# Kernel optimization log

Hardware: AMD Instinct MI355X
Metric: run time of the kernel (lower is better)

The kernel has to match this reference:

```python
import jax, jax.numpy as jnp
import numpy as np

B, I, D = 16384, 128, 16  # batch, input_size, n_dim


def setup_inputs() -> dict:
    key = jax.random.key(0)
    ks = jax.random.split(key, 14)
    inp = {
        "h": jax.random.normal(ks[0], (B, I * D), dtype=jnp.float32),
        "X": jax.random.normal(ks[1], (B, I), dtype=jnp.float32),
        "M": jax.random.uniform(ks[2], (B, I), dtype=jnp.float32),
        "gamma_h": jax.random.uniform(ks[3], (B, I, D), dtype=jnp.float32),
        "W_r": jax.random.normal(ks[4], (I, 1, D), dtype=jnp.float32),
        "W_z": jax.random.normal(ks[5], (I, 1, D), dtype=jnp.float32),
        "W_h": jax.random.normal(ks[6], (I, 1, D), dtype=jnp.float32),
        "U_r": jax.random.normal(ks[7], (I, D, D), dtype=jnp.float32),
        "U_z": jax.random.normal(ks[8], (I, D, D), dtype=jnp.float32),
        "U_h": jax.random.normal(ks[9], (I, D, D), dtype=jnp.float32),
        "V_r": jax.random.normal(ks[10], (I, 1, D), dtype=jnp.float32),
        "V_z": jax.random.normal(ks[11], (I, 1, D), dtype=jnp.float32),
        "V_h": jax.random.normal(ks[12], (I, 1, D), dtype=jnp.float32),
        "b_r": jnp.zeros((I, D), dtype=jnp.float32),
        "b_z": jnp.zeros((I, D), dtype=jnp.float32),
        "b_h": jnp.zeros((I, D), dtype=jnp.float32),
    }
    return inp


def reference(h, X, M, gamma_h, W_r, W_z, W_h, U_r, U_z, U_h,
              V_r, V_z, V_h, b_r, b_z, b_h):
    b = X.shape[0]
    i, d = W_r.shape[0], W_r.shape[2]
    # decayed hidden state, per-feature blocks: [B, I, D]
    hh = h.reshape(b, i, d) * gamma_h
    # X/M contributions: X is [B, I]; W/V are [I, 1, D] -> outer product per feature
    xr = jnp.einsum('bi,id->bid', X, W_r[:, 0, :])
    xz = jnp.einsum('bi,id->bid', X, W_z[:, 0, :])
    xh = jnp.einsum('bi,id->bid', X, W_h[:, 0, :])
    mr = jnp.einsum('bi,id->bid', M, V_r[:, 0, :])
    mz = jnp.einsum('bi,id->bid', M, V_z[:, 0, :])
    mh = jnp.einsum('bi,id->bid', M, V_h[:, 0, :])
    # per-feature small matmuls on hidden blocks
    r = jax.nn.sigmoid(xr + jnp.einsum('bid,ide->bie', hh, U_r) + mr + b_r)
    z = jax.nn.sigmoid(xz + jnp.einsum('bid,ide->bie', hh, U_z) + mz + b_z)
    h_tilde = jnp.tanh(xh + jnp.einsum('bid,ide->bie', r * hh, U_h) + mh + b_h)
    out = z * hh + (1.0 - z) * h_tilde
    return out.reshape(b, i * d)
```

## Files before the change

kernel.cpp:

```cpp
#include <hip/hip_runtime.h>
#include <hip/hip_bf16.h>


typedef float  f32x4_t  __attribute__((ext_vector_type(4)));
typedef short  bf16x8_t __attribute__((ext_vector_type(8)));

constexpr int I_TOT = 128;
constexpr int ROWL  = 2048;
constexpr int SW    = 260;

__device__ __forceinline__ unsigned short bf16c(float x) {
    union { __hip_bfloat16 b; unsigned short u; } cv;
    cv.b = __float2bfloat16(x);
    return cv.u;
}
__device__ __forceinline__ float bf16_to_f(unsigned short b) {
    union { float f; unsigned u; } c; c.u = ((unsigned)b) << 16;
    return c.f;
}
__device__ __forceinline__ float fast_sigmoid(float x) {
    float e = __expf(-x);
    return __builtin_amdgcn_rcpf(1.0f + e);
}
__device__ __forceinline__ float fast_tanh(float x) {
    x = fminf(fmaxf(x, -10.0f), 10.0f);
    float e = __expf(-2.0f * x);
    return (1.0f - e) * __builtin_amdgcn_rcpf(1.0f + e);
}

__device__ __forceinline__ bf16x8_t build_a(float a0, float a1, float a2, float a3) {
    unsigned short h0 = bf16c(a0), h1 = bf16c(a1),
                   h2 = bf16c(a2), h3 = bf16c(a3);
    unsigned short l0 = bf16c(a0 - bf16_to_f(h0));
    unsigned short l1 = bf16c(a1 - bf16_to_f(h1));
    unsigned short l2 = bf16c(a2 - bf16_to_f(h2));
    unsigned short l3 = bf16c(a3 - bf16_to_f(h3));
    bf16x8_t A;
    A[0] = (short)h0; A[1] = (short)h1; A[2] = (short)h2; A[3] = (short)h3;
    A[4] = (short)l0; A[5] = (short)l1; A[6] = (short)l2; A[7] = (short)l3;
    return A;
}

__device__ __forceinline__ bf16x8_t build_u(float u0, float u1, float u2, float u3) {
    unsigned short h0 = bf16c(u0), h1 = bf16c(u1),
                   h2 = bf16c(u2), h3 = bf16c(u3);
    bf16x8_t B;
    B[0] = (short)h0; B[1] = (short)h1; B[2] = (short)h2; B[3] = (short)h3;
    B[4] = (short)h0; B[5] = (short)h1; B[6] = (short)h2; B[7] = (short)h3;
    return B;
}

__device__ __forceinline__ f32x4_t mm(bf16x8_t a, bf16x8_t b, f32x4_t c) {
    return __builtin_amdgcn_mfma_f32_16x16x32_bf16(a, b, c, 0, 0, 0);
}

__global__ __launch_bounds__(256)
__attribute__((amdgpu_waves_per_eu(4, 8)))
void gru_d_mfma(
    const float* __restrict__ h,
    const float* __restrict__ X,
    const float* __restrict__ M,
    const float* __restrict__ gam,
    const float* __restrict__ W_r, const float* __restrict__ W_z, const float* __restrict__ W_h,
    const float* __restrict__ U_r, const float* __restrict__ U_z, const float* __restrict__ U_h,
    const float* __restrict__ V_r, const float* __restrict__ V_z, const float* __restrict__ V_h,
    const float* __restrict__ b_r, const float* __restrict__ b_z, const float* __restrict__ b_h,
    float* __restrict__ out)
{
    __shared__ __align__(16) float shh[16 * SW];

    const int t  = threadIdx.x;
    const int w  = t >> 6;
    const int l  = t & 63;
    const int bi = l & 15;
    const int dA = (l >> 4) * 4;

    const int b0 = blockIdx.y * 16;
    const int i0 = blockIdx.x * 16;

    {
        const int r0 = 4 * w;
#define STAGE(rr)                                                             \
        {                                                                     \
            const size_t gb = (size_t)(b0 + r0 + (rr)) * ROWL + i0 * 16;      \
            float4 hv = *reinterpret_cast<const float4*>(h   + gb + 4 * l);   \
            float4 gv = *reinterpret_cast<const float4*>(gam + gb + 4 * l);   \
            float4 p;                                                         \
            p.x = hv.x * gv.x; p.y = hv.y * gv.y;                             \
            p.z = hv.z * gv.z; p.w = hv.w * gv.w;                             \
            *reinterpret_cast<float4*>(&shh[(r0 + (rr)) * SW + 4 * l]) = p;   \
        }
        STAGE(0) STAGE(1) STAGE(2) STAGE(3)
#undef STAGE
    }
    __syncthreads();

    const int iw0 = i0 + w * 4;
    const size_t orow = (size_t)(b0 + bi) * ROWL + dA;
    const size_t xrow = (size_t)(b0 + bi) * I_TOT;

    float4 phh = *reinterpret_cast<const float4*>(&shh[bi * SW + (w * 4) * 16 + dA]);
    float px = X[xrow + iw0];
    float pm = M[xrow + iw0];
    const float* Urp = U_r + iw0 * 256 + bi;
    const float* Uzp = U_z + iw0 * 256 + bi;
    const float* Uhp = U_h + iw0 * 256 + bi;
    float pur0 = Urp[(dA+0)*16], pur1 = Urp[(dA+1)*16],
          pur2 = Urp[(dA+2)*16], pur3 = Urp[(dA+3)*16];
    float puz0 = Uzp[(dA+0)*16], puz1 = Uzp[(dA+1)*16],
          puz2 = Uzp[(dA+2)*16], puz3 = Uzp[(dA+3)*16];
    float puh0 = Uhp[(dA+0)*16], puh1 = Uhp[(dA+1)*16],
          puh2 = Uhp[(dA+2)*16], puh3 = Uhp[(dA+3)*16];

    #pragma unroll
    for (int it = 0; it < 4; ++it) {
        const int i = iw0 + it;

        const float4 wr4 = *reinterpret_cast<const float4*>(W_r + i*16 + dA);
        const float4 wz4 = *reinterpret_cast<const float4*>(W_z + i*16 + dA);
        const float4 wh4 = *reinterpret_cast<const float4*>(W_h + i*16 + dA);
        const float4 vr4 = *reinterpret_cast<const float4*>(V_r + i*16 + dA);
        const float4 vz4 = *reinterpret_cast<const float4*>(V_z + i*16 + dA);
        const float4 vh4 = *reinterpret_cast<const float4*>(V_h + i*16 + dA);
        const float4 br4 = *reinterpret_cast<const float4*>(b_r + i*16 + dA);
        const float4 bz4 = *reinterpret_cast<const float4*>(b_z + i*16 + dA);
        const float4 bh4 = *reinterpret_cast<const float4*>(b_h + i*16 + dA);

        bf16x8_t BUr = build_u(pur0, pur1, pur2, pur3);
        bf16x8_t BUz = build_u(puz0, puz1, puz2, puz3);
        bf16x8_t BUh = build_u(puh0, puh1, puh2, puh3);

        float hh0 = phh.x, hh1 = phh.y, hh2 = phh.z, hh3 = phh.w;
        bf16x8_t Ahh = build_a(hh0, hh1, hh2, hh3);

        float4 nhh; float nx, nm;
        float nur0, nur1, nur2, nur3, nuz0, nuz1, nuz2, nuz3, nuh0, nuh1, nuh2, nuh3;
        if (it < 3) {
            const int ipf = i + 1;
            nhh = *reinterpret_cast<const float4*>(
                &shh[bi * SW + (w * 4 + it + 1) * 16 + dA]);
            nx = X[xrow + ipf];
            nm = M[xrow + ipf];
            const float* nUr = U_r + ipf * 256 + bi;
            const float* nUz = U_z + ipf * 256 + bi;
            const float* nUh = U_h + ipf * 256 + bi;
            nur0 = nUr[(dA+0)*16]; nur1 = nUr[(dA+1)*16];
            nur2 = nUr[(dA+2)*16]; nur3 = nUr[(dA+3)*16];
            nuz0 = nUz[(dA+0)*16]; nuz1 = nUz[(dA+1)*16];
            nuz2 = nUz[(dA+2)*16]; nuz3 = nUz[(dA+3)*16];
            nuh0 = nUh[(dA+0)*16]; nuh1 = nUh[(dA+1)*16];
            nuh2 = nUh[(dA+2)*16]; nuh3 = nUh[(dA+3)*16];
        }

        f32x4_t initR, initZ, initH;
        initR[0] = fmaf(px, wr4.x, fmaf(pm, vr4.x, br4.x));
        initR[1] = fmaf(px, wr4.y, fmaf(pm, vr4.y, br4.y));
        initR[2] = fmaf(px, wr4.z, fmaf(pm, vr4.z, br4.z));
        initR[3] = fmaf(px, wr4.w, fmaf(pm, vr4.w, br4.w));
        initZ[0] = fmaf(px, wz4.x, fmaf(pm, vz4.x, bz4.x));
        initZ[1] = fmaf(px, wz4.y, fmaf(pm, vz4.y, bz4.y));
        initZ[2] = fmaf(px, wz4.z, fmaf(pm, vz4.z, bz4.z));
        initZ[3] = fmaf(px, wz4.w, fmaf(pm, vz4.w, bz4.w));
        f32x4_t accR = mm(BUr, Ahh, initR);
        f32x4_t accZ = mm(BUz, Ahh, initZ);

        float rh0 = fast_sigmoid(accR[0]) * hh0;
        float rh1 = fast_sigmoid(accR[1]) * hh1;
        float rh2 = fast_sigmoid(accR[2]) * hh2;
        float rh3 = fast_sigmoid(accR[3]) * hh3;
        bf16x8_t Arh = build_a(rh0, rh1, rh2, rh3);

        initH[0] = fmaf(px, wh4.x, fmaf(pm, vh4.x, bh4.x));
        initH[1] = fmaf(px, wh4.y, fmaf(pm, vh4.y, bh4.y));
        initH[2] = fmaf(px, wh4.z, fmaf(pm, vh4.z, bh4.z));
        initH[3] = fmaf(px, wh4.w, fmaf(pm, vh4.w, bh4.w));
        f32x4_t accH = mm(BUh, Arh, initH);

        float4 o;
        {
            float z0 = fast_sigmoid(accZ[0]); float t0 = fast_tanh(accH[0]);
            o.x = fmaf(z0, hh0 - t0, t0);
            float z1 = fast_sigmoid(accZ[1]); float t1 = fast_tanh(accH[1]);
            o.y = fmaf(z1, hh1 - t1, t1);
            float z2 = fast_sigmoid(accZ[2]); float t2 = fast_tanh(accH[2]);
            o.z = fmaf(z2, hh2 - t2, t2);
            float z3 = fast_sigmoid(accZ[3]); float t3 = fast_tanh(accH[3]);
            o.w = fmaf(z3, hh3 - t3, t3);
        }
        *reinterpret_cast<float4*>(out + orow + (size_t)i * 16) = o;

        if (it < 3) {
            phh = nhh; px = nx; pm = nm;
            pur0 = nur0; pur1 = nur1; pur2 = nur2; pur3 = nur3;
            puz0 = nuz0; puz1 = nuz1; puz2 = nuz2; puz3 = nuz3;
            puh0 = nuh0; puh1 = nuh1; puh2 = nuh2; puh3 = nuh3;
        }
    }
}

extern "C" void kernel_launch(void* const* d_in, const int* in_sizes, int n_in,
                              void* d_out, int out_size, void* d_ws, size_t ws_size,
                              hipStream_t stream) {
    const float* h       = (const float*)d_in[0];
    const float* X       = (const float*)d_in[1];
    const float* M       = (const float*)d_in[2];
    const float* gamma_h = (const float*)d_in[3];
    const float* W_r     = (const float*)d_in[4];
    const float* W_z     = (const float*)d_in[5];
    const float* W_h     = (const float*)d_in[6];
    const float* U_r     = (const float*)d_in[7];
    const float* U_z     = (const float*)d_in[8];
    const float* U_h     = (const float*)d_in[9];
    const float* V_r     = (const float*)d_in[10];
    const float* V_z     = (const float*)d_in[11];
    const float* V_h     = (const float*)d_in[12];
    const float* b_r     = (const float*)d_in[13];
    const float* b_z     = (const float*)d_in[14];
    const float* b_h     = (const float*)d_in[15];
    float* out = (float*)d_out;

    dim3 grid(I_TOT / 16, 16384 / 16);
    dim3 block(256);
    gru_d_mfma<<<grid, block, 0, stream>>>(h, X, M, gamma_h,
                                           W_r, W_z, W_h,
                                           U_r, U_z, U_h,
                                           V_r, V_z, V_h,
                                           b_r, b_z, b_h,
                                           out);
}
```

Baseline: 113.0 us.

## Loop blocks over batch tiles with double-buffered async LDS loads and staged stores

The grid shrinks to 128 blocks along the batch axis, and each block now walks 8 batch tiles. The next tile's h and gamma rows are prefetched into a second LDS buffer with global_load_lds while the current tile is computed. The h*gamma product moves from staging to the compute loop. Outputs are written back into LDS and then stored to global memory as contiguous rows, so stores are coalesced. This trades parallelism and occupancy (fewer blocks, more LDS per block) for overlap of loads with compute and fewer partial-line writes, and it relies on the barrier waiting for the async LDS loads to finish.

```diff
diff --git a/kernel.cpp b/kernel.cpp
--- a/kernel.cpp
+++ b/kernel.cpp
@@ -8,6 +8,13 @@
 constexpr int I_TOT = 128;
 constexpr int ROWL  = 2048;
 constexpr int SW    = 260;
+constexpr int NTK   = 8;
+constexpr int YB    = 128;
+
+#define GLD16(gsrc, ldst)                                                     \
+    __builtin_amdgcn_global_load_lds(                                         \
+        (const __attribute__((address_space(1))) void*)(gsrc),                \
+        (__attribute__((address_space(3))) void*)(ldst), 16, 0, 0)
 
 __device__ __forceinline__ unsigned short bf16c(float x) {
     union { __hip_bfloat16 b; unsigned short u; } cv;
@@ -55,7 +62,6 @@
 }
 
 __global__ __launch_bounds__(256)
-__attribute__((amdgpu_waves_per_eu(4, 8)))
 void gru_d_mfma(
     const float* __restrict__ h,
     const float* __restrict__ X,
@@ -67,134 +73,161 @@
     const float* __restrict__ b_r, const float* __restrict__ b_z, const float* __restrict__ b_h,
     float* __restrict__ out)
 {
-    __shared__ __align__(16) float shh[16 * SW];
+    __shared__ __align__(16) float sh[2][16 * SW];
+    __shared__ __align__(16) float sg[2][16 * SW];
 
     const int t  = threadIdx.x;
     const int w  = t >> 6;
     const int l  = t & 63;
     const int bi = l & 15;
     const int dA = (l >> 4) * 4;
-
-    const int b0 = blockIdx.y * 16;
-    const int i0 = blockIdx.x * 16;
+    const int r0 = 4 * w;
+
+    const int i0  = blockIdx.x * 16;
+    const int iw0 = i0 + w * 4;
 
     {
-        const int r0 = 4 * w;
-#define STAGE(rr)                                                             \
-        {                                                                     \
-            const size_t gb = (size_t)(b0 + r0 + (rr)) * ROWL + i0 * 16;      \
-            float4 hv = *reinterpret_cast<const float4*>(h   + gb + 4 * l);   \
-            float4 gv = *reinterpret_cast<const float4*>(gam + gb + 4 * l);   \
-            float4 p;                                                         \
-            p.x = hv.x * gv.x; p.y = hv.y * gv.y;                             \
-            p.z = hv.z * gv.z; p.w = hv.w * gv.w;                             \
-            *reinterpret_cast<float4*>(&shh[(r0 + (rr)) * SW + 4 * l]) = p;   \
-        }
-        STAGE(0) STAGE(1) STAGE(2) STAGE(3)
-#undef STAGE
+        const size_t b0p = (size_t)blockIdx.y * 16;
+        #pragma unroll
+        for (int rr = 0; rr < 4; ++rr) {
+            const size_t gb = (b0p + r0 + rr) * ROWL + i0 * 16;
+            GLD16(h   + gb + 4 * l, &sh[0][(r0 + rr) * SW]);
+            GLD16(gam + gb + 4 * l, &sg[0][(r0 + rr) * SW]);
+        }
     }
-    __syncthreads();
-
-    const int iw0 = i0 + w * 4;
-    const size_t orow = (size_t)(b0 + bi) * ROWL + dA;
-    const size_t xrow = (size_t)(b0 + bi) * I_TOT;
-
-    float4 phh = *reinterpret_cast<const float4*>(&shh[bi * SW + (w * 4) * 16 + dA]);
-    float px = X[xrow + iw0];
-    float pm = M[xrow + iw0];
-    const float* Urp = U_r + iw0 * 256 + bi;
-    const float* Uzp = U_z + iw0 * 256 + bi;
-    const float* Uhp = U_h + iw0 * 256 + bi;
-    float pur0 = Urp[(dA+0)*16], pur1 = Urp[(dA+1)*16],
-          pur2 = Urp[(dA+2)*16], pur3 = Urp[(dA+3)*16];
-    float puz0 = Uzp[(dA+0)*16], puz1 = Uzp[(dA+1)*16],
-          puz2 = Uzp[(dA+2)*16], puz3 = Uzp[(dA+3)*16];
-    float puh0 = Uhp[(dA+0)*16], puh1 = Uhp[(dA+1)*16],
-          puh2 = Uhp[(dA+2)*16], puh3 = Uhp[(dA+3)*16];
-
-    #pragma unroll
-    for (int it = 0; it < 4; ++it) {
-        const int i = iw0 + it;
-
-        const float4 wr4 = *reinterpret_cast<const float4*>(W_r + i*16 + dA);
-        const float4 wz4 = *reinterpret_cast<const float4*>(W_z + i*16 + dA);
-        const float4 wh4 = *reinterpret_cast<const float4*>(W_h + i*16 + dA);
-        const float4 vr4 = *reinterpret_cast<const float4*>(V_r + i*16 + dA);
-        const float4 vz4 = *reinterpret_cast<const float4*>(V_z + i*16 + dA);
-        const float4 vh4 = *reinterpret_cast<const float4*>(V_h + i*16 + dA);
-        const float4 br4 = *reinterpret_cast<const float4*>(b_r + i*16 + dA);
-        const float4 bz4 = *reinterpret_cast<const float4*>(b_z + i*16 + dA);
-        const float4 bh4 = *reinterpret_cast<const float4*>(b_h + i*16 + dA);
-
-        bf16x8_t BUr = build_u(pur0, pur1, pur2, pur3);
-        bf16x8_t BUz = build_u(puz0, puz1, puz2, puz3);
-        bf16x8_t BUh = build_u(puh0, puh1, puh2, puh3);
-
-        float hh0 = phh.x, hh1 = phh.y, hh2 = phh.z, hh3 = phh.w;
-        bf16x8_t Ahh = build_a(hh0, hh1, hh2, hh3);
-
-        float4 nhh; float nx, nm;
-        float nur0, nur1, nur2, nur3, nuz0, nuz1, nuz2, nuz3, nuh0, nuh1, nuh2, nuh3;
-        if (it < 3) {
-            const int ipf = i + 1;
-            nhh = *reinterpret_cast<const float4*>(
-                &shh[bi * SW + (w * 4 + it + 1) * 16 + dA]);
-            nx = X[xrow + ipf];
-            nm = M[xrow + ipf];
-            const float* nUr = U_r + ipf * 256 + bi;
-            const float* nUz = U_z + ipf * 256 + bi;
-            const float* nUh = U_h + ipf * 256 + bi;
-            nur0 = nUr[(dA+0)*16]; nur1 = nUr[(dA+1)*16];
-            nur2 = nUr[(dA+2)*16]; nur3 = nUr[(dA+3)*16];
-            nuz0 = nUz[(dA+0)*16]; nuz1 = nUz[(dA+1)*16];
-            nuz2 = nUz[(dA+2)*16]; nuz3 = nUz[(dA+3)*16];
-            nuh0 = nUh[(dA+0)*16]; nuh1 = nUh[(dA+1)*16];
-            nuh2 = nUh[(dA+2)*16]; nuh3 = nUh[(dA+3)*16];
-        }
-
-        f32x4_t initR, initZ, initH;
-        initR[0] = fmaf(px, wr4.x, fmaf(pm, vr4.x, br4.x));
-        initR[1] = fmaf(px, wr4.y, fmaf(pm, vr4.y, br4.y));
-        initR[2] = fmaf(px, wr4.z, fmaf(pm, vr4.z, br4.z));
-        initR[3] = fmaf(px, wr4.w, fmaf(pm, vr4.w, br4.w));
-        initZ[0] = fmaf(px, wz4.x, fmaf(pm, vz4.x, bz4.x));
-        initZ[1] = fmaf(px, wz4.y, fmaf(pm, vz4.y, bz4.y));
-        initZ[2] = fmaf(px, wz4.z, fmaf(pm, vz4.z, bz4.z));
-        initZ[3] = fmaf(px, wz4.w, fmaf(pm, vz4.w, bz4.w));
-        f32x4_t accR = mm(BUr, Ahh, initR);
-        f32x4_t accZ = mm(BUz, Ahh, initZ);
-
-        float rh0 = fast_sigmoid(accR[0]) * hh0;
-        float rh1 = fast_sigmoid(accR[1]) * hh1;
-        float rh2 = fast_sigmoid(accR[2]) * hh2;
-        float rh3 = fast_sigmoid(accR[3]) * hh3;
-        bf16x8_t Arh = build_a(rh0, rh1, rh2, rh3);
-
-        initH[0] = fmaf(px, wh4.x, fmaf(pm, vh4.x, bh4.x));
-        initH[1] = fmaf(px, wh4.y, fmaf(pm, vh4.y, bh4.y));
-        initH[2] = fmaf(px, wh4.z, fmaf(pm, vh4.z, bh4.z));
-        initH[3] = fmaf(px, wh4.w, fmaf(pm, vh4.w, bh4.w));
-        f32x4_t accH = mm(BUh, Arh, initH);
-
-        float4 o;
-        {
-            float z0 = fast_sigmoid(accZ[0]); float t0 = fast_tanh(accH[0]);
-            o.x = fmaf(z0, hh0 - t0, t0);
-            float z1 = fast_sigmoid(accZ[1]); float t1 = fast_tanh(accH[1]);
-            o.y = fmaf(z1, hh1 - t1, t1);
-            float z2 = fast_sigmoid(accZ[2]); float t2 = fast_tanh(accH[2]);
-            o.z = fmaf(z2, hh2 - t2, t2);
-            float z3 = fast_sigmoid(accZ[3]); float t3 = fast_tanh(accH[3]);
-            o.w = fmaf(z3, hh3 - t3, t3);
-        }
-        *reinterpret_cast<float4*>(out + orow + (size_t)i * 16) = o;
-
-        if (it < 3) {
-            phh = nhh; px = nx; pm = nm;
-            pur0 = nur0; pur1 = nur1; pur2 = nur2; pur3 = nur3;
-            puz0 = nuz0; puz1 = nuz1; puz2 = nuz2; puz3 = nuz3;
-            puh0 = nuh0; puh1 = nuh1; puh2 = nuh2; puh3 = nuh3;
-        }
+
+    int cur = 0;
+    #pragma unroll 1
+    for (int k = 0; k < NTK; ++k) {
+        __syncthreads();
+        const int b0 = (blockIdx.y + k * YB) * 16;
+        float* sbh = sh[cur];
+        float* sbg = sg[cur];
+
+        if (k < NTK - 1) {
+            const size_t nb0 = (size_t)(blockIdx.y + (k + 1) * YB) * 16;
+            #pragma unroll
+            for (int rr = 0; rr < 4; ++rr) {
+                const size_t gb = (nb0 + r0 + rr) * ROWL + i0 * 16;
+                GLD16(h   + gb + 4 * l, &sh[cur ^ 1][(r0 + rr) * SW]);
+                GLD16(gam + gb + 4 * l, &sg[cur ^ 1][(r0 + rr) * SW]);
+            }
+        }
+
+        const size_t xrow = (size_t)(b0 + bi) * I_TOT;
+
+        float4 phv = *reinterpret_cast<const float4*>(&sbh[bi * SW + (w * 4) * 16 + dA]);
+        float4 pgv = *reinterpret_cast<const float4*>(&sbg[bi * SW + (w * 4) * 16 + dA]);
+        float px = X[xrow + iw0];
+        float pm = M[xrow + iw0];
+        const float* Urp = U_r + iw0 * 256 + bi;
+        const float* Uzp = U_z + iw0 * 256 + bi;
+        const float* Uhp = U_h + iw0 * 256 + bi;
+        float pur0 = Urp[(dA+0)*16], pur1 = Urp[(dA+1)*16],
+              pur2 = Urp[(dA+2)*16], pur3 = Urp[(dA+3)*16];
+        float puz0 = Uzp[(dA+0)*16], puz1 = Uzp[(dA+1)*16],
+              puz2 = Uzp[(dA+2)*16], puz3 = Uzp[(dA+3)*16];
+        float puh0 = Uhp[(dA+0)*16], puh1 = Uhp[(dA+1)*16],
+              puh2 = Uhp[(dA+2)*16], puh3 = Uhp[(dA+3)*16];
+
+        #pragma unroll
+        for (int it = 0; it < 4; ++it) {
+            const int i = iw0 + it;
+
+            const float4 wr4 = *reinterpret_cast<const float4*>(W_r + i*16 + dA);
+            const float4 wz4 = *reinterpret_cast<const float4*>(W_z + i*16 + dA);
+            const float4 wh4 = *reinterpret_cast<const float4*>(W_h + i*16 + dA);
+            const float4 vr4 = *reinterpret_cast<const float4*>(V_r + i*16 + dA);
+            const float4 vz4 = *reinterpret_cast<const float4*>(V_z + i*16 + dA);
+            const float4 vh4 = *reinterpret_cast<const float4*>(V_h + i*16 + dA);
+            const float4 br4 = *reinterpret_cast<const float4*>(b_r + i*16 + dA);
+            const float4 bz4 = *reinterpret_cast<const float4*>(b_z + i*16 + dA);
+            const float4 bh4 = *reinterpret_cast<const float4*>(b_h + i*16 + dA);
+
+            bf16x8_t BUr = build_u(pur0, pur1, pur2, pur3);
+            bf16x8_t BUz = build_u(puz0, puz1, puz2, puz3);
+            bf16x8_t BUh = build_u(puh0, puh1, puh2, puh3);
+
+            const float hh0 = phv.x * pgv.x, hh1 = phv.y * pgv.y,
+                        hh2 = phv.z * pgv.z, hh3 = phv.w * pgv.w;
+            bf16x8_t Ahh = build_a(hh0, hh1, hh2, hh3);
+
+            float4 nhv, ngv; float nx, nm;
+            float nur0, nur1, nur2, nur3, nuz0, nuz1, nuz2, nuz3,
+                  nuh0, nuh1, nuh2, nuh3;
+            if (it < 3) {
+                const int ipf = i + 1;
+                nhv = *reinterpret_cast<const float4*>(
+                    &sbh[bi * SW + (w * 4 + it + 1) * 16 + dA]);
+                ngv = *reinterpret_cast<const float4*>(
+                    &sbg[bi * SW + (w * 4 + it + 1) * 16 + dA]);
+                nx = X[xrow + ipf];
+                nm = M[xrow + ipf];
+                const float* nUr = U_r + ipf * 256 + bi;
+                const float* nUz = U_z + ipf * 256 + bi;
+                const float* nUh = U_h + ipf * 256 + bi;
+                nur0 = nUr[(dA+0)*16]; nur1 = nUr[(dA+1)*16];
+                nur2 = nUr[(dA+2)*16]; nur3 = nUr[(dA+3)*16];
+                nuz0 = nUz[(dA+0)*16]; nuz1 = nUz[(dA+1)*16];
+                nuz2 = nUz[(dA+2)*16]; nuz3 = nUz[(dA+3)*16];
+                nuh0 = nUh[(dA+0)*16]; nuh1 = nUh[(dA+1)*16];
+                nuh2 = nUh[(dA+2)*16]; nuh3 = nUh[(dA+3)*16];
+            }
+
+            f32x4_t initR, initZ, initH;
+            initR[0] = fmaf(px, wr4.x, fmaf(pm, vr4.x, br4.x));
+            initR[1] = fmaf(px, wr4.y, fmaf(pm, vr4.y, br4.y));
+            initR[2] = fmaf(px, wr4.z, fmaf(pm, vr4.z, br4.z));
+            initR[3] = fmaf(px, wr4.w, fmaf(pm, vr4.w, br4.w));
+            initZ[0] = fmaf(px, wz4.x, fmaf(pm, vz4.x, bz4.x));
+            initZ[1] = fmaf(px, wz4.y, fmaf(pm, vz4.y, bz4.y));
+            initZ[2] = fmaf(px, wz4.z, fmaf(pm, vz4.z, bz4.z));
+            initZ[3] = fmaf(px, wz4.w, fmaf(pm, vz4.w, bz4.w));
+            f32x4_t accR = mm(BUr, Ahh, initR);
+            f32x4_t accZ = mm(BUz, Ahh, initZ);
+
+            float rh0 = fast_sigmoid(accR[0]) * hh0;
+            float rh1 = fast_sigmoid(accR[1]) * hh1;
+            float rh2 = fast_sigmoid(accR[2]) * hh2;
+            float rh3 = fast_sigmoid(accR[3]) * hh3;
+            bf16x8_t Arh = build_a(rh0, rh1, rh2, rh3);
+
+            initH[0] = fmaf(px, wh4.x, fmaf(pm, vh4.x, bh4.x));
+            initH[1] = fmaf(px, wh4.y, fmaf(pm, vh4.y, bh4.y));
+            initH[2] = fmaf(px, wh4.z, fmaf(pm, vh4.z, bh4.z));
+            initH[3] = fmaf(px, wh4.w, fmaf(pm, vh4.w, bh4.w));
+            f32x4_t accH = mm(BUh, Arh, initH);
+
+            float4 o;
+            {
+                float z0 = fast_sigmoid(accZ[0]); float t0 = fast_tanh(accH[0]);
+                o.x = fmaf(z0, hh0 - t0, t0);
+                float z1 = fast_sigmoid(accZ[1]); float t1 = fast_tanh(accH[1]);
+                o.y = fmaf(z1, hh1 - t1, t1);
+                float z2 = fast_sigmoid(accZ[2]); float t2 = fast_tanh(accH[2]);
+                o.z = fmaf(z2, hh2 - t2, t2);
+                float z3 = fast_sigmoid(accZ[3]); float t3 = fast_tanh(accH[3]);
+                o.w = fmaf(z3, hh3 - t3, t3);
+            }
+            *reinterpret_cast<float4*>(&sbh[bi * SW + (w * 4 + it) * 16 + dA]) = o;
+
+            if (it < 3) {
+                phv = nhv; pgv = ngv; px = nx; pm = nm;
+                pur0 = nur0; pur1 = nur1; pur2 = nur2; pur3 = nur3;
+                puz0 = nuz0; puz1 = nuz1; puz2 = nuz2; puz3 = nuz3;
+                puh0 = nuh0; puh1 = nuh1; puh2 = nuh2; puh3 = nuh3;
+            }
+        }
+        __syncthreads();
+
+        #pragma unroll
+        for (int rr = 0; rr < 4; ++rr) {
+            const size_t gb = (size_t)(b0 + r0 + rr) * ROWL + i0 * 16;
+            float4 v = *reinterpret_cast<const float4*>(&sbh[(r0 + rr) * SW + 4 * l]);
+            *reinterpret_cast<float4*>(out + gb + 4 * l) = v;
+        }
+
+        cur ^= 1;
     }
 }
 
@@ -219,7 +252,7 @@
     const float* b_h     = (const float*)d_in[15];
     float* out = (float*)d_out;
 
-    dim3 grid(I_TOT / 16, 16384 / 16);
+    dim3 grid(I_TOT / 16, YB);
     dim3 block(256);
     gru_d_mfma<<<grid, block, 0, stream>>>(h, X, M, gamma_h,
                                            W_r, W_z, W_h,
```

Result: slower. 119.0 us (+5.3%).
